# Kernel tuning notes

Hardware: AMD Instinct MI355X
Metric: run time of the kernel (lower is better)

## Reference

```python
import jax, jax.numpy as jnp
import numpy as np

B, T, D = 4, 2048, 2048
K, D_B, TOPK, WINDOW = 7, 128, 16, 64
GATE_CAP = 1.0
STRAND_CAP = 1.0
_PHI = 1.618033988749895
_PSI = -0.6180339887498949


def _ln(x, g, b, eps=1e-5):
    m = jnp.mean(x, axis=-1, keepdims=True)
    v = jnp.mean((x - m) ** 2, axis=-1, keepdims=True)
    return (x - m) * jax.lax.rsqrt(v + eps) * g + b


def setup_inputs() -> dict:
    ks = jax.random.split(jax.random.key(0), 20)
    rn = lambda k, s, sc=1.0: jax.random.normal(k, s, jnp.float32) * sc
    d_s = 1.0 / np.sqrt(D)
    db_s = 1.0 / np.sqrt(D_B)
    return {
        'X_write': rn(ks[0], (B, T, D)),
        'X_read': rn(ks[1], (B, T, D)),
        'slots': rn(ks[2], (B, K, D_B)),
        'W0': rn(ks[3], (D, D), d_s),
        'ln_write_g': jnp.ones((D,), jnp.float32),
        'ln_write_b': jnp.zeros((D,), jnp.float32),
        'Wv': rn(ks[4], (D_B, D), d_s),
        'Wk': rn(ks[5], (D_B, D_B), db_s),
        'slot_key_bias': rn(ks[6], (K, D_B), 2.0),
        'Wg_w': rn(ks[7], (D_B, 2 * D_B), 1.0 / np.sqrt(2 * D_B)),
        'Wg_b': jnp.full((D_B,), -2.0, jnp.float32),
        'ln_strand_g': jnp.ones((D_B,), jnp.float32),
        'ln_strand_b': jnp.zeros((D_B,), jnp.float32),
        'Wsq': rn(ks[8], (D_B, D_B), db_s),
        'Wsk': rn(ks[9], (D_B, D_B), db_s),
        'Wsv': rn(ks[10], (D_B, D_B), db_s),
        'lambda_strand': rn(ks[11], (D_B,), 0.1),
        'Wq_read': rn(ks[12], (D_B, D), d_s),
        'Wk_read': rn(ks[13], (D_B, D_B), db_s),
        'Wv_read': rn(ks[14], (D, D_B), db_s),
        'render_coeffs': rn(ks[15], (K, 3, D), 0.1),
        'slot_temps': 1.0 + rn(ks[16], (K,), 0.1),
    }


def reference(X_write, X_read, slots, W0, ln_write_g, ln_write_b, Wv, Wk,
              slot_key_bias, Wg_w, Wg_b, ln_strand_g, ln_strand_b,
              Wsq, Wsk, Wsv, lambda_strand, Wq_read, Wk_read, Wv_read,
              render_coeffs, slot_temps):
    b, t, d = X_write.shape
    sd = 1.0 / np.sqrt(D_B)
    X_n = _ln(X_write, ln_write_g, ln_write_b)

    # --- banded salience + topk (torch.no_grad region; only int indices escape) ---
    W_eff = min(WINDOW, t - 1)
    Xs = jax.lax.stop_gradient(X_n)
    X_W0 = Xs @ jax.lax.stop_gradient(W0).T            # [b,t,d]
    Xp = jnp.pad(X_W0, ((0, 0), (W_eff, 0), (0, 0)))   # left-pad so offset w -> j = i + w - W

    def band_dot(w):
        return jnp.einsum('btd,btd->bt', Xs,
                          jax.lax.dynamic_slice_in_dim(Xp, w, t, axis=1))

    band = jax.vmap(band_dot)(jnp.arange(W_eff)).transpose(1, 2, 0)  # [b,t,W]
    ii = jnp.arange(t)[:, None]
    ww = jnp.arange(W_eff)[None, :]
    jj = ii + ww - W_eff
    valid = (jj >= 0) & (ii >= 1)                      # j in [max(0,i-W), i)
    sal = jnp.where(valid, band, -jnp.inf).reshape(b, -1)
    topk_eff = min(TOPK, t * (t - 1) // 2)
    _, idx = jax.lax.top_k(sal, topk_eff)              # [b,topk]
    i_idx = idx // W_eff
    j_idx = i_idx + (idx % W_eff) - W_eff

    # --- topk pair gather + bilinear relation ---
    x_new = jnp.take_along_axis(X_n, i_idx[..., None], axis=1)  # [b,topk,d]
    x_old = jnp.take_along_axis(X_n, j_idx[..., None], axis=1)
    pair_sal = jnp.sum(x_new * (x_old @ jax.lax.stop_gradient(W0).T), axis=-1)
    alpha = jax.nn.softmax(pair_sal, axis=-1)
    R_t = jnp.einsum('bp,bpe->be', alpha, (x_new - x_old) @ Wv.T)  # [b,d_b]

    # --- slot write ---
    slot_keys = slots @ Wk.T + slot_key_bias[None]
    compat = jnp.einsum('bke,be->bk', slot_keys, R_t) * sd
    compat = compat * jax.nn.softplus(slot_temps)[None]
    sw = jax.nn.softmax(compat, axis=-1)
    weighted_R = sw[..., None] * R_t[:, None, :]                 # [b,K,d_b]
    g = jax.nn.sigmoid(jnp.concatenate([slots, weighted_R], -1) @ Wg_w.T + Wg_b)
    slots_upd = (1.0 - g) * slots + g * weighted_R

    # --- strand mixer (KxK self-attention) ---
    B_ln = _ln(slots_upd, ln_strand_g, ln_strand_b)
    att = jax.nn.softmax(jnp.einsum('bke,bme->bkm', B_ln @ Wsq.T, B_ln @ Wsk.T) * sd, axis=-1)
    ctx = att @ (B_ln @ Wsv.T)
    slots_next = slots_upd + ctx * jnp.clip(jnp.tanh(lambda_strand), -STRAND_CAP, STRAND_CAP)

    # --- aux losses ---
    L_persist = jnp.mean((slots_next - slots) ** 2)
    nrm = jnp.linalg.norm(slots_next, axis=-1, keepdims=True)
    Bn = slots_next / jnp.maximum(nrm, 1e-12)
    cos = jnp.einsum('bke,bme->bkm', Bn, Bn)
    off = 1.0 - jnp.eye(K, dtype=cos.dtype)
    L_div = jnp.sum(cos ** 2 * off) / (b * K * (K - 1))

    # --- directional render gate + read ---
    q_r = X_read @ Wq_read.T                    # [b,t,d_b]
    k_r = slots_next @ Wk_read.T                # [b,K,d_b]
    v_r = slots_next @ Wv_read.T                # [b,K,d]
    scores = jnp.einsum('bte,bke->btk', q_r, k_r) * sd
    q_mean = jnp.mean(X_read, axis=1)           # [b,d]
    w0q = q_mean @ jax.lax.stop_gradient(W0).T
    dphi = _PHI - _PSI
    phi_q = (w0q - _PSI * q_mean) / dphi
    psi_q = (_PHI * q_mean - w0q) / dphi
    pm = jnp.linalg.norm(phi_q, axis=-1, keepdims=True)
    sm = jnp.linalg.norm(psi_q, axis=-1, keepdims=True)
    tot = pm + sm + 1e-6
    basis = jnp.concatenate([jnp.ones_like(pm), pm / tot, sm / tot], axis=-1)  # [b,3]
    gate = jnp.clip(jnp.tanh(jnp.einsum('bi,kid->bkd', basis, render_coeffs)),
                    -GATE_CAP, GATE_CAP)
    z = jnp.einsum('btk,bkd->btd', jax.nn.softmax(scores, axis=-1), v_r * gate)
    return z, slots_next, L_persist, L_div
```

## Files before the change

kernel.cpp:

```cpp
#include <hip/hip_runtime.h>
#include <cstdint>
#include <cstddef>

#define DEV __device__ __forceinline__

typedef __bf16 bf16x8 __attribute__((ext_vector_type(8)));
typedef float f32x4 __attribute__((ext_vector_type(4)));
typedef unsigned short u16;
typedef unsigned int u32;

constexpr int Bq = 4, Tq = 2048, Dq = 2048, Kq = 7, DB = 128, TK = 16;
constexpr float SD = 0.08838834764831845f;
constexpr float PHIc = 1.618033988749895f;
constexpr float PSIc = -0.6180339887498949f;
constexpr float DPHI = 2.2360679774997896f;
#define NEG_INF (-__builtin_inff())

DEV u16 f2bf(float f) {
  union { float f; u32 u; } x; x.f = f;
  u32 r = (x.u + 0x7fffu + ((x.u >> 16) & 1u)) >> 16;
  return (u16)r;
}
DEV float bfbits2f(u32 h) { union { u32 u; float f; } x; x.u = h << 16; return x.f; }

DEV void async16(void* l, const void* g) {
  __builtin_amdgcn_global_load_lds((const __attribute__((address_space(1))) void*)g,
                                   (__attribute__((address_space(3))) void*)l, 16, 0, 0);
}

__global__ __launch_bounds__(256) void k_prep(const float* __restrict__ W0, u16* __restrict__ W0b,
                                              const float* __restrict__ Xw, const float* __restrict__ g,
                                              const float* __restrict__ bb, u16* __restrict__ Xn,
                                              const float* __restrict__ Xr, float* __restrict__ part) {
  int bid = blockIdx.x;
  int tid = threadIdx.x;
  if (bid < 2048) {
    size_t i = ((size_t)bid * 256 + tid) * 8;
    float4 a = *(const float4*)&W0[i];
    float4 c = *(const float4*)&W0[i + 4];
    u32 p0 = (u32)f2bf(a.x) | ((u32)f2bf(a.y) << 16);
    u32 p1 = (u32)f2bf(a.z) | ((u32)f2bf(a.w) << 16);
    u32 p2 = (u32)f2bf(c.x) | ((u32)f2bf(c.y) << 16);
    u32 p3 = (u32)f2bf(c.z) | ((u32)f2bf(c.w) << 16);
    uint4 st; st.x = p0; st.y = p1; st.z = p2; st.w = p3;
    *(uint4*)&W0b[i] = st;
  } else if (bid < 2048 + 8192) {
    int row = bid - 2048;
    const float* xr = Xw + (size_t)row * Dq;
    int lane = tid & 63, w = tid >> 6;
    float4 a = *(const float4*)&xr[tid * 8];
    float4 c = *(const float4*)&xr[tid * 8 + 4];
    float s = a.x + a.y + a.z + a.w + c.x + c.y + c.z + c.w;
    float q = a.x*a.x + a.y*a.y + a.z*a.z + a.w*a.w + c.x*c.x + c.y*c.y + c.z*c.z + c.w*c.w;
    #pragma unroll
    for (int o = 32; o; o >>= 1) { s += __shfl_xor(s, o); q += __shfl_xor(q, o); }
    __shared__ float red[8];
    if (lane == 0) { red[w] = s; red[w + 4] = q; }
    __syncthreads();
    float S = red[0] + red[1] + red[2] + red[3];
    float Q = red[4] + red[5] + red[6] + red[7];
    float mean = S * (1.0f / Dq);
    float var = Q * (1.0f / Dq) - mean * mean;
    float rstd = rsqrtf(var + 1e-5f);
    float v[8] = {a.x, a.y, a.z, a.w, c.x, c.y, c.z, c.w};
    u32 p[4];
    #pragma unroll
    for (int j = 0; j < 4; ++j) {
      int d0 = tid * 8 + j * 2;
      float o0 = (v[j*2]   - mean) * rstd * g[d0]   + bb[d0];
      float o1 = (v[j*2+1] - mean) * rstd * g[d0+1] + bb[d0+1];
      p[j] = (u32)f2bf(o0) | ((u32)f2bf(o1) << 16);
    }
    uint4 st; st.x = p[0]; st.y = p[1]; st.z = p[2]; st.w = p[3];
    *(uint4*)&Xn[(size_t)row * Dq + tid * 8] = st;
  } else {
    int f = bid - (2048 + 8192);
    int s = f & 1, y = (f >> 1) & 31, b = f >> 6;
    const float* xb = Xr + (size_t)b * Tq * Dq + (size_t)s * 1024 + tid * 4;
    f32x4 acc = {0.f, 0.f, 0.f, 0.f};
    #pragma unroll 4
    for (int t = 0; t < 64; ++t) {
      const float4 v = *(const float4*)&xb[(size_t)(y * 64 + t) * Dq];
      acc[0] += v.x; acc[1] += v.y; acc[2] += v.z; acc[3] += v.w;
    }
    float4 st; st.x = acc[0]; st.y = acc[1]; st.z = acc[2]; st.w = acc[3];
    *(float4*)&part[((size_t)(b * 32 + y)) * Dq + s * 1024 + tid * 4] = st;
  }
}

__global__ __launch_bounds__(256) void k_qmean2(const float* __restrict__ part, float* __restrict__ qm) {
  int s = blockIdx.x, b = blockIdx.y, tid = threadIdx.x;
  int col = s * 1024 + tid * 4;
  f32x4 acc = {0.f, 0.f, 0.f, 0.f};
  #pragma unroll 8
  for (int y = 0; y < 32; ++y) {
    float4 v = *(const float4*)&part[((size_t)(b * 32 + y)) * Dq + col];
    acc[0] += v.x; acc[1] += v.y; acc[2] += v.z; acc[3] += v.w;
  }
  float4 st;
  st.x = acc[0] * (1.0f / Tq); st.y = acc[1] * (1.0f / Tq);
  st.z = acc[2] * (1.0f / Tq); st.w = acc[3] * (1.0f / Tq);
  *(float4*)&qm[(size_t)b * Dq + col] = st;
}

__global__ __launch_bounds__(256) void k_w0q(const float* __restrict__ W0, const float* __restrict__ qm,
                                             float* __restrict__ w0q) {
  __shared__ float qs[4][Dq];
  int tid = threadIdx.x, lane = tid & 63, w = tid >> 6;
  for (int i = tid * 4; i < 4 * Dq; i += 1024) {
    *(float4*)&((float*)qs)[i] = *(const float4*)&qm[i];
  }
  __syncthreads();
  #pragma unroll
  for (int r = 0; r < 2; ++r) {
    int d = blockIdx.x * 8 + w * 2 + r;
    const float* wr = W0 + (size_t)d * Dq;
    float a0 = 0, a1 = 0, a2 = 0, a3 = 0;
    for (int e = lane * 4; e < Dq; e += 256) {
      float4 wv = *(const float4*)&wr[e];
      float4 q0 = *(const float4*)&qs[0][e];
      float4 q1 = *(const float4*)&qs[1][e];
      float4 q2 = *(const float4*)&qs[2][e];
      float4 q3 = *(const float4*)&qs[3][e];
      a0 += wv.x*q0.x + wv.y*q0.y + wv.z*q0.z + wv.w*q0.w;
      a1 += wv.x*q1.x + wv.y*q1.y + wv.z*q1.z + wv.w*q1.w;
      a2 += wv.x*q2.x + wv.y*q2.y + wv.z*q2.z + wv.w*q2.w;
      a3 += wv.x*q3.x + wv.y*q3.y + wv.z*q3.z + wv.w*q3.w;
    }
    #pragma unroll
    for (int o = 32; o; o >>= 1) {
      a0 += __shfl_xor(a0, o); a1 += __shfl_xor(a1, o);
      a2 += __shfl_xor(a2, o); a3 += __shfl_xor(a3, o);
    }
    if (lane == 0) {
      w0q[0 * Dq + d] = a0; w0q[1 * Dq + d] = a1;
      w0q[2 * Dq + d] = a2; w0q[3 * Dq + d] = a3;
    }
  }
}

__global__ __launch_bounds__(256) void k_basis(const float* __restrict__ qm, const float* __restrict__ w0q,
                                               float* __restrict__ basis) {
  int b = blockIdx.x, tid = threadIdx.x;
  __shared__ float red[256];
  __shared__ float psum;
  float ps = 0, ss = 0;
  for (int d = tid; d < Dq; d += 256) {
    float qv = qm[b * Dq + d], wv = w0q[b * Dq + d];
    float ph = (wv - PSIc * qv) * (1.0f / DPHI);
    float pv = (PHIc * qv - wv) * (1.0f / DPHI);
    ps += ph * ph; ss += pv * pv;
  }
  red[tid] = ps; __syncthreads();
  for (int st = 128; st; st >>= 1) { if (tid < st) red[tid] += red[tid + st]; __syncthreads(); }
  if (tid == 0) psum = red[0];
  __syncthreads();
  red[tid] = ss; __syncthreads();
  for (int st = 128; st; st >>= 1) { if (tid < st) red[tid] += red[tid + st]; __syncthreads(); }
  if (tid == 0) {
    float pm = sqrtf(psum), sm = sqrtf(red[0]);
    float tot = pm + sm + 1e-6f;
    basis[b * 3 + 0] = 1.0f; basis[b * 3 + 1] = pm / tot; basis[b * 3 + 2] = sm / tot;
  }
}

__global__ __launch_bounds__(256) void k_gemm(const u16* __restrict__ A, const u16* __restrict__ B,
                                              u16* __restrict__ C, int M, int N, int K) {
  __shared__ u16 As[128 * 64], Bs[128 * 64];
  int tid = threadIdx.x, lane = tid & 63, w = tid >> 6, wr = w >> 1, wc = w & 1;
  int bm = blockIdx.x, bn = blockIdx.y;
  const u16* Ab = A + (size_t)bm * 128 * K;
  const u16* Bb = B + (size_t)bn * 128 * K;
  f32x4 zero = {0.f, 0.f, 0.f, 0.f};
  f32x4 acc[4][4];
  #pragma unroll
  for (int mi = 0; mi < 4; ++mi)
    #pragma unroll
    for (int ni = 0; ni < 4; ++ni) acc[mi][ni] = zero;
  int ro = tid >> 3;
  int co = (tid & 7) * 8;
  int cs = co ^ ((ro & 7) * 8);
  for (int k0 = 0; k0 < K; k0 += 64) {
    #pragma unroll
    for (int i = 0; i < 4; ++i) {
      int row = ro + i * 32;
      async16(&As[row * 64 + co], Ab + (size_t)row * K + k0 + cs);
      async16(&Bs[row * 64 + co], Bb + (size_t)row * K + k0 + cs);
    }
    __syncthreads();
    #pragma unroll
    for (int ks = 0; ks < 2; ++ks) {
      int cbase = ks * 32 + ((lane >> 4) * 8);
      int crd = cbase ^ ((lane & 7) * 8);
      bf16x8 af[4], bfr[4];
      #pragma unroll
      for (int mi = 0; mi < 4; ++mi)
        af[mi] = *(const bf16x8*)&As[(wr * 64 + mi * 16 + (lane & 15)) * 64 + crd];
      #pragma unroll
      for (int ni = 0; ni < 4; ++ni)
        bfr[ni] = *(const bf16x8*)&Bs[(wc * 64 + ni * 16 + (lane & 15)) * 64 + crd];
      #pragma unroll
      for (int mi = 0; mi < 4; ++mi)
        #pragma unroll
        for (int ni = 0; ni < 4; ++ni)
          acc[mi][ni] = __builtin_amdgcn_mfma_f32_16x16x32_bf16(af[mi], bfr[ni], acc[mi][ni], 0, 0, 0);
    }
    __syncthreads();
  }
  int r0 = bm * 128 + wr * 64, c0 = bn * 128 + wc * 64;
  #pragma unroll
  for (int mi = 0; mi < 4; ++mi)
    #pragma unroll
    for (int ni = 0; ni < 4; ++ni) {
      int col = c0 + ni * 16 + (lane & 15);
      int rb = r0 + mi * 16 + ((lane >> 4) * 4);
      #pragma unroll
      for (int rg = 0; rg < 4; ++rg)
        C[(size_t)(rb + rg) * N + col] = f2bf(acc[mi][ni][rg]);
    }
}

__global__ __launch_bounds__(768) void k_band(const u16* __restrict__ Xn, const u16* __restrict__ XW0,
                                              float* __restrict__ sal) {
  int b = blockIdx.y, i0 = blockIdx.x * 32;
  int tid = threadIdx.x, lane = tid & 63, w = tid >> 6;
  int mi = w / 6, ni = w % 6;
  const u16* Xb = Xn + (size_t)b * Tq * Dq;
  const u16* Wb = XW0 + (size_t)b * Tq * Dq;
  int koff = (lane >> 4) * 8;
  const u16* ap = Xb + (size_t)(i0 + mi * 16 + (lane & 15)) * Dq + koff;
  int j = i0 - 64 + ni * 16 + (lane & 15); j = min(max(j, 0), Tq - 1);
  const u16* bp = Wb + (size_t)j * Dq + koff;
  f32x4 zero = {0.f, 0.f, 0.f, 0.f};
  f32x4 accA = zero, accB = zero;
  for (int k = 0; k < Dq; k += 64) {
    bf16x8 a0 = *(const bf16x8*)(ap + k);
    bf16x8 b0 = *(const bf16x8*)(bp + k);
    bf16x8 a1 = *(const bf16x8*)(ap + k + 32);
    bf16x8 b1 = *(const bf16x8*)(bp + k + 32);
    accA = __builtin_amdgcn_mfma_f32_16x16x32_bf16(a0, b0, accA, 0, 0, 0);
    accB = __builtin_amdgcn_mfma_f32_16x16x32_bf16(a1, b1, accB, 0, 0, 0);
  }
  int nl = ni * 16 + (lane & 15);
  #pragma unroll
  for (int rg = 0; rg < 4; ++rg) {
    int i = i0 + mi * 16 + (lane >> 4) * 4 + rg;
    int wb = nl - (i - i0);
    if (wb >= 0 && wb < 64) {
      int jj = i0 - 64 + nl;
      bool valid = (jj >= 0) && (i >= 1);
      sal[((size_t)b * Tq + i) * 64 + wb] = valid ? (accA[rg] + accB[rg]) : NEG_INF;
    }
  }
}

__global__ __launch_bounds__(256) void k_topk1(const float* __restrict__ sal,
                                               float* __restrict__ cv, int* __restrict__ ci) {
  int b = blockIdx.y, chunk = blockIdx.x;
  int tid = threadIdx.x, lane = tid & 63;
  const float* s = sal + (size_t)b * Tq * 64 + (size_t)chunk * 1024;
  float lv[4]; int li[4];
  #pragma unroll
  for (int i = 0; i < 4; ++i) { lv[i] = NEG_INF; li[i] = -1; }
  #pragma unroll
  for (int i = 0; i < 4; ++i) {
    int e = tid + i * 256;
    float v = s[e];
    int idx = chunk * 1024 + e;
    if (v > lv[3]) {
      lv[3] = v; li[3] = idx;
      #pragma unroll
      for (int q = 3; q > 0; --q)
        if (lv[q] > lv[q - 1]) {
          float tv = lv[q]; lv[q] = lv[q - 1]; lv[q - 1] = tv;
          int t2 = li[q]; li[q] = li[q - 1]; li[q - 1] = t2;
        }
    }
  }
  __shared__ float Sv[256][4];
  __shared__ int Si[256][4];
  __shared__ int heads[256];
  #pragma unroll
  for (int i = 0; i < 4; ++i) { Sv[tid][i] = lv[i]; Si[tid][i] = li[i]; }
  heads[tid] = 0;
  __syncthreads();
  float* ov = cv + ((size_t)b * 128 + chunk) * 16;
  int* oi = ci + ((size_t)b * 128 + chunk) * 16;
  for (int r = 0; r < 16; ++r) {
    if (tid < 64) {
      float best = NEG_INF; int bl = 0; int bidx = 0x7fffffff;
      #pragma unroll
      for (int cc = 0; cc < 4; ++cc) {
        int c = lane + cc * 64;
        int h = heads[c];
        float v = (h < 4) ? Sv[c][h] : NEG_INF;
        int ix = (h < 4) ? Si[c][h] : 0x7fffffff;
        if (v > best || (v == best && ix < bidx)) { best = v; bl = c; bidx = ix; }
      }
      #pragma unroll
      for (int o = 32; o; o >>= 1) {
        float bv = __shfl_xor(best, o); int blx = __shfl_xor(bl, o); int bix = __shfl_xor(bidx, o);
        if (bv > best || (bv == best && bix < bidx)) { best = bv; bl = blx; bidx = bix; }
      }
      if (lane == 0) {
        int h = heads[bl];
        ov[r] = best; oi[r] = (h < 4) ? Si[bl][h] : -1;
        heads[bl] = h + 1;
      }
    }
    __syncthreads();
  }
}

__global__ __launch_bounds__(256) void k_topk2(const float* __restrict__ cv, const int* __restrict__ ci,
                                               int* __restrict__ ti, int* __restrict__ tj) {
  int b = blockIdx.x, tid = threadIdx.x, lane = tid & 63;
  __shared__ float Sv[128][16];
  __shared__ int Si[128][16];
  __shared__ int heads[128];
  __shared__ int ridx[16];
  for (int i = tid; i < 128 * 16; i += 256) {
    ((float*)Sv)[i] = cv[(size_t)b * 2048 + i];
    ((int*)Si)[i] = ci[(size_t)b * 2048 + i];
  }
  if (tid < 128) heads[tid] = 0;
  __syncthreads();
  for (int r = 0; r < 16; ++r) {
    if (tid < 64) {
      float best = NEG_INF; int bl = 0; int bidx = 0x7fffffff;
      #pragma unroll
      for (int cc = 0; cc < 2; ++cc) {
        int c = lane + cc * 64;
        int h = heads[c];
        float v = (h < 16) ? Sv[c][h] : NEG_INF;
        int ix = (h < 16) ? Si[c][h] : 0x7fffffff;
        if (v > best || (v == best && ix < bidx)) { best = v; bl = c; bidx = ix; }
      }
      #pragma unroll
      for (int o = 32; o; o >>= 1) {
        float bv = __shfl_xor(best, o); int blx = __shfl_xor(bl, o); int bix = __shfl_xor(bidx, o);
        if (bv > best || (bv == best && bix < bidx)) { best = bv; bl = blx; bidx = bix; }
      }
// ... 52 lines not shown
}

__global__ __launch_bounds__(256) void k_pairsal(const float* __restrict__ W0, const float* __restrict__ Xnew,
                                                 const float* __restrict__ Xold, float* __restrict__ psal) {
  int d0 = blockIdx.x * 64, e0 = blockIdx.y * 64;
  int tid = threadIdx.x, P = tid & 63, dg = tid >> 6;
  f32x4 xo[16];
  #pragma unroll
  for (int i = 0; i < 16; ++i)
    xo[i] = *(const f32x4*)&Xold[(size_t)P * Dq + e0 + i * 4];
  int dbase = d0 + dg * 16;
  f32x4 xn[4];
  #pragma unroll
  for (int i = 0; i < 4; ++i)
    xn[i] = *(const f32x4*)&Xnew[(size_t)P * Dq + dbase + i * 4];
  float acc = 0.f;
  #pragma unroll
  for (int dd = 0; dd < 16; ++dd) {
    int d = __builtin_amdgcn_readfirstlane(dbase + dd);
    const float* wr = W0 + (size_t)d * Dq + e0;
    float i0 = 0.f, i1 = 0.f, i2 = 0.f, i3 = 0.f;
    #pragma unroll
    for (int i = 0; i < 16; ++i) {
      float4 wv = *(const float4*)&wr[i * 4];
      i0 += wv.x * xo[i][0]; i1 += wv.y * xo[i][1];
      i2 += wv.z * xo[i][2]; i3 += wv.w * xo[i][3];
    }
    acc += xn[dd >> 2][dd & 3] * ((i0 + i1) + (i2 + i3));
  }
  __shared__ float part[4][64];
  part[dg][P] = acc;
  __syncthreads();
  if (tid < 64)
    atomicAdd(&psal[tid], part[0][tid] + part[1][tid] + part[2][tid] + part[3][tid]);
}

__global__ __launch_bounds__(256) void k_alphart(const float* __restrict__ psal, const float* __restrict__ Xnew,
    const float* __restrict__ Xold, const float* __restrict__ Wv, float* __restrict__ Rt) {
  int bx = blockIdx.x, b = blockIdx.y;
  int tid = threadIdx.x, lane = tid & 63, w = tid >> 6;
  __shared__ float al[16], xd[Dq];
  if (tid == 0) {
    float mx = NEG_INF;
    #pragma unroll
    for (int p = 0; p < 16; ++p) mx = fmaxf(mx, psal[b * 16 + p]);
    float ee[16]; float s = 0.f;
    #pragma unroll
    for (int p = 0; p < 16; ++p) { ee[p] = expf(psal[b * 16 + p] - mx); s += ee[p]; }
    #pragma unroll
    for (int p = 0; p < 16; ++p) al[p] = ee[p] / s;
  }
  __syncthreads();
  {
    int d0 = tid * 8;
    float a8[8] = {0, 0, 0, 0, 0, 0, 0, 0};
    #pragma unroll
    for (int p = 0; p < 16; ++p) {
      const float* xn = Xnew + (size_t)(b * 16 + p) * Dq + d0;
      const float* xo = Xold + (size_t)(b * 16 + p) * Dq + d0;
      float ap = al[p];
      float4 n0 = *(const float4*)xn;
      float4 n1 = *(const float4*)(xn + 4);
      float4 o0 = *(const float4*)xo;
      float4 o1 = *(const float4*)(xo + 4);
      a8[0] += ap * (n0.x - o0.x); a8[1] += ap * (n0.y - o0.y);
      a8[2] += ap * (n0.z - o0.z); a8[3] += ap * (n0.w - o0.w);
      a8[4] += ap * (n1.x - o1.x); a8[5] += ap * (n1.y - o1.y);
      a8[6] += ap * (n1.z - o1.z); a8[7] += ap * (n1.w - o1.w);
    }
    #pragma unroll
    for (int j = 0; j < 8; ++j) xd[d0 + j] = a8[j];
  }
  __syncthreads();
  int e = bx * 4 + w;
  const float* wr = Wv + (size_t)e * Dq;
  float s = 0.f;
  #pragma unroll 8
  for (int d = lane; d < Dq; d += 64) s += wr[d] * xd[d];
  #pragma unroll
  for (int o = 32; o; o >>= 1) s += __shfl_xor(s, o);
  if (lane == 0) Rt[b * DB + e] = s;
}

__global__ __launch_bounds__(256) void ksl_a(const float* __restrict__ slots, const float* __restrict__ Wk,
    const float* __restrict__ skb, const float* __restrict__ Rt, const float* __restrict__ temps,
    float* __restrict__ compat) {
  int k = blockIdx.x, b = blockIdx.y;
  int tid = threadIdx.x, g = tid >> 4, sub = tid & 15;
  __shared__ float s_s[DB], r_s[DB], sk_s[DB];
  if (tid < DB) { s_s[tid] = slots[((size_t)(b * Kq + k)) * DB + tid]; r_s[tid] = Rt[b * DB + tid]; }
  __syncthreads();
  #pragma unroll
  for (int r = 0; r < 8; ++r) {
    int e = g * 8 + r;
    const float* wr = Wk + e * DB;
    float a = 0.f;
    #pragma unroll
    for (int j = 0; j < 8; ++j) a += wr[sub + j * 16] * s_s[sub + j * 16];
    a += __shfl_xor(a, 8); a += __shfl_xor(a, 4); a += __shfl_xor(a, 2); a += __shfl_xor(a, 1);
    if (sub == 0) sk_s[e] = a + skb[k * DB + e];
  }
  __syncthreads();
  if (tid < 64) {
    float a = sk_s[tid] * r_s[tid] + sk_s[tid + 64] * r_s[tid + 64];
    #pragma unroll
    for (int o = 32; o; o >>= 1) a += __shfl_xor(a, o);
    if (tid == 0) {
      float t = temps[k];
      compat[b * Kq + k] = a * SD * log1pf(expf(t));
    }
  }
}

__global__ __launch_bounds__(256) void ksl_c(const float* __restrict__ slots, const float* __restrict__ Rt,
    const float* __restrict__ compat, const float* __restrict__ Wgw, const float* __restrict__ Wgb,
    const float* __restrict__ lng, const float* __restrict__ lnb,
    const float* __restrict__ Wsq, const float* __restrict__ Wsk, const float* __restrict__ Wsv,
    float* __restrict__ suOut, float* __restrict__ qqOut, float* __restrict__ kkOut,
    float* __restrict__ vvOut) {
  int k = blockIdx.x, b = blockIdx.y;
  int tid = threadIdx.x, g = tid >> 4, sub = tid & 15;
  __shared__ float s_s[DB], r_s[DB], su[DB], bnl[DB];
  __shared__ float mvm, mvr;
  if (tid < DB) { s_s[tid] = slots[((size_t)(b * Kq + k)) * DB + tid]; r_s[tid] = Rt[b * DB + tid]; }
  __syncthreads();
  float swk;
  {
    float cm[Kq]; float mx = NEG_INF;
    #pragma unroll
    for (int kk = 0; kk < Kq; ++kk) { cm[kk] = compat[b * Kq + kk]; mx = fmaxf(mx, cm[kk]); }
    float ssum = 0.f;
    #pragma unroll
    for (int kk = 0; kk < Kq; ++kk) { cm[kk] = expf(cm[kk] - mx); ssum += cm[kk]; }
    swk = cm[k] / ssum;
  }
  #pragma unroll
  for (int r = 0; r < 8; ++r) {
    int e = g * 8 + r;
    const float* wr = Wgw + e * 256;
    float a = 0.f;
    #pragma unroll
    for (int j = 0; j < 16; ++j) {
      int col = sub + j * 16;
      float x = (j < 8) ? s_s[col] : swk * r_s[col - 128];
      a += wr[col] * x;
    }
    a += __shfl_xor(a, 8); a += __shfl_xor(a, 4); a += __shfl_xor(a, 2); a += __shfl_xor(a, 1);
    if (sub == 0) {
      a += Wgb[e];
      float gv = 1.0f / (1.0f + expf(-a));
      float wrv = swk * r_s[e];
      su[e] = (1.0f - gv) * s_s[e] + gv * wrv;
    }
  }
  __syncthreads();
  if (tid < 64) {
    float v0 = su[tid], v1 = su[tid + 64];
    float s = v0 + v1, q = v0 * v0 + v1 * v1;
    #pragma unroll
    for (int o = 32; o; o >>= 1) { s += __shfl_xor(s, o); q += __shfl_xor(q, o); }
    if (tid == 0) {
      float m = s / DB; float va = q / DB - m * m;
      mvm = m; mvr = rsqrtf(va + 1e-5f);
    }
  }
  __syncthreads();
  if (tid < DB) {
    bnl[tid] = (su[tid] - mvm) * mvr * lng[tid] + lnb[tid];
    suOut[((size_t)(b * Kq + k)) * DB + tid] = su[tid];
  }
  __syncthreads();
  #pragma unroll
  for (int r = 0; r < 8; ++r) {
    int e = g * 8 + r;
    const float* wr1 = Wsq + e * DB;
    const float* wr2 = Wsk + e * DB;
    const float* wr3 = Wsv + e * DB;
    float a1 = 0.f, a2 = 0.f, a3 = 0.f;
    #pragma unroll
    for (int j = 0; j < 8; ++j) {
      float x = bnl[sub + j * 16];
      a1 += wr1[sub + j * 16] * x;
      a2 += wr2[sub + j * 16] * x;
      a3 += wr3[sub + j * 16] * x;
    }
    #pragma unroll
    for (int o = 8; o; o >>= 1) {
      a1 += __shfl_xor(a1, o); a2 += __shfl_xor(a2, o); a3 += __shfl_xor(a3, o);
    }
    if (sub == 0) {
      size_t oi = ((size_t)(b * Kq + k)) * DB + e;
      qqOut[oi] = a1; kkOut[oi] = a2; vvOut[oi] = a3;
    }
  }
}

__global__ __launch_bounds__(256) void ksl_d(const float* __restrict__ suOut, const float* __restrict__ qqOut,
    const float* __restrict__ kkOut, const float* __restrict__ vvOut, const float* __restrict__ lam,
    const float* __restrict__ Wkr, float* __restrict__ snOut, float* __restrict__ krOut) {
  int k = blockIdx.x, b = blockIdx.y;
  int tid = threadIdx.x, g = tid >> 4, sub = tid & 15;
  __shared__ float qq[DB], kks[Kq][DB], vvs[Kq][DB], att[8], sn_s[DB];
  if (tid < DB) qq[tid] = qqOut[((size_t)(b * Kq + k)) * DB + tid];
  for (int i = tid; i < Kq * DB; i += 256) {
    ((float*)kks)[i] = kkOut[(size_t)b * Kq * DB + i];
    ((float*)vvs)[i] = vvOut[(size_t)b * Kq * DB + i];
  }
  __syncthreads();
  if (tid < 112) {
    int m = g;
    float a = 0.f;
    #pragma unroll
    for (int j = 0; j < 8; ++j) a += qq[sub + j * 16] * kks[m][sub + j * 16];
    a += __shfl_xor(a, 8); a += __shfl_xor(a, 4); a += __shfl_xor(a, 2); a += __shfl_xor(a, 1);
    if (sub == 0) att[m] = a * SD;
  }
  __syncthreads();
  if (tid == 0) {
    float mx = att[0];
    for (int m = 1; m < Kq; ++m) mx = fmaxf(mx, att[m]);
    float s = 0.f;
    for (int m = 0; m < Kq; ++m) { att[m] = expf(att[m] - mx); s += att[m]; }
    for (int m = 0; m < Kq; ++m) att[m] /= s;
  }
  __syncthreads();
  if (tid < DB) {
    float c = 0.f;
    #pragma unroll
    for (int m = 0; m < Kq; ++m) c += att[m] * vvs[m][tid];
    float l = tanhf(lam[tid]); l = fminf(fmaxf(l, -1.0f), 1.0f);
    float v = suOut[((size_t)(b * Kq + k)) * DB + tid] + c * l;
    sn_s[tid] = v;
    snOut[((size_t)(b * Kq + k)) * DB + tid] = v;
  }
  __syncthreads();
  #pragma unroll
  for (int r = 0; r < 8; ++r) {
    int e = g * 8 + r;
    const float* wr = Wkr + e * DB;
    float a = 0.f;
    #pragma unroll
    for (int j = 0; j < 8; ++j) a += wr[sub + j * 16] * sn_s[sub + j * 16];
    a += __shfl_xor(a, 8); a += __shfl_xor(a, 4); a += __shfl_xor(a, 2); a += __shfl_xor(a, 1);
    if (sub == 0) krOut[((size_t)(b * Kq + k)) * DB + e] = a;
  }
}

__global__ __launch_bounds__(256) void k_mvg(const float* __restrict__ snOut, const float* __restrict__ krOut,
    const float* __restrict__ Wqr, const float* __restrict__ Wvr, const float* __restrict__ rc,
    const float* __restrict__ basis, const float* __restrict__ slots,
    u16* __restrict__ Mb, u16* __restrict__ Vgb, float* __restrict__ out2) {
  int b = blockIdx.y, tid = threadIdx.x;
  if (blockIdx.x == 8) {
    if (b != 0) return;
    __shared__ float red[256];
    __shared__ float nrm[28];
    float p = 0.f;
    for (int i = tid; i < Bq * Kq * DB; i += 256) { float d = snOut[i] - slots[i]; p += d * d; }
    red[tid] = p; __syncthreads();
    for (int st = 128; st; st >>= 1) { if (tid < st) red[tid] += red[tid + st]; __syncthreads(); }
    if (tid == 0) out2[0] = red[0] / (float)(Bq * Kq * DB);
    if (tid < 28) {
      int bb2 = tid / 7, k = tid % 7;
      float s = 0.f;
      for (int e = 0; e < DB; ++e) { float v = snOut[(size_t)(bb2 * 7 + k) * DB + e]; s += v * v; }
      nrm[tid] = fmaxf(sqrtf(s), 1e-12f);
    }
    __syncthreads();
    float dv = 0.f;
    if (tid < 168) {
      int bb2 = tid / 42, r = tid % 42;
      int k = r / 6, m = r % 6; m += (m >= k);
      float dot = 0.f;
      for (int e = 0; e < DB; ++e)
        dot += snOut[(size_t)(bb2 * 7 + k) * DB + e] * snOut[(size_t)(bb2 * 7 + m) * DB + e];
      float c = dot / (nrm[bb2 * 7 + k] * nrm[bb2 * 7 + m]);
      dv = c * c;
    }
    red[tid] = dv; __syncthreads();
    for (int st = 128; st; st >>= 1) { if (tid < st) red[tid] += red[tid + st]; __syncthreads(); }
    if (tid == 0) out2[1] = red[0] / 168.0f;
    return;
  }
  int d = blockIdx.x * 256 + tid;
  __shared__ float krs[Kq][DB], sns[Kq][DB];
  for (int i = tid; i < Kq * DB; i += 256) {
    ((float*)krs)[i] = krOut[(size_t)b * Kq * DB + i];
    ((float*)sns)[i] = snOut[(size_t)b * Kq * DB + i];
  }
  __syncthreads();
  float b0 = basis[b * 3 + 0], b1 = basis[b * 3 + 1], b2 = basis[b * 3 + 2];
  float am[7] = {0, 0, 0, 0, 0, 0, 0};
  for (int e = 0; e < DB; ++e) {
    float wq = Wqr[(size_t)e * Dq + d];
    #pragma unroll
    for (int k = 0; k < 7; ++k) am[k] += krs[k][e] * wq;
  }
  float vr[7] = {0, 0, 0, 0, 0, 0, 0};
  const float* wvrow = Wvr + (size_t)d * DB;
  for (int e = 0; e < DB; ++e) {
    float wv = wvrow[e];
    #pragma unroll
    for (int k = 0; k < 7; ++k) vr[k] += sns[k][e] * wv;
  }
  #pragma unroll
  for (int k = 0; k < 7; ++k) {
    Mb[((size_t)b * 7 + k) * Dq + d] = f2bf(am[k]);
    float gt = tanhf(b0 * rc[((size_t)k * 3 + 0) * Dq + d] +
                     b1 * rc[((size_t)k * 3 + 1) * Dq + d] +
                     b2 * rc[((size_t)k * 3 + 2) * Dq + d]);
    gt = fminf(fmaxf(gt, -1.0f), 1.0f);
    Vgb[((size_t)b * 7 + k) * Dq + d] = f2bf(vr[k] * gt);
  }
}
// ... 22 lines not shown
    #pragma unroll
    for (int k = 0; k < 7; ++k) {
      #pragma unroll
      for (int o = 32; o; o >>= 1) sc[k] += __shfl_xor(sc[k], o);
    }
    float mx = sc[0];
    #pragma unroll
    for (int k = 1; k < 7; ++k) mx = fmaxf(mx, sc[k]);
    float pz[7]; float s = 0.f;
    #pragma unroll
    for (int k = 0; k < 7; ++k) { pz[k] = expf((sc[k] - mx) * SD); s += pz[k]; }
    float inv = 1.0f / s;
    #pragma unroll
    for (int k = 0; k < 7; ++k) pz[k] *= inv;
    float* zr = Z + ((size_t)b * Tq + t) * Dq;
    #pragma unroll
    for (int i = 0; i < 8; ++i) {
      int d = lane * 4 + i * 256;
      float4 o4; o4.x = o4.y = o4.z = o4.w = 0.f;
      #pragma unroll
      for (int k = 0; k < 7; ++k) {
        uint2 vm = *(const uint2*)&Vs[k * 2048 + d];
        float pk = pz[k];
        o4.x += pk * bfbits2f(vm.x & 0xffffu); o4.y += pk * bfbits2f(vm.x >> 16);
        o4.z += pk * bfbits2f(vm.y & 0xffffu); o4.w += pk * bfbits2f(vm.y >> 16);
      }
      *(float4*)&zr[d] = o4;
    }
  }
}

extern "C" void kernel_launch(void* const* d_in, const int* in_sizes, int n_in,
                              void* d_out, int out_size, void* d_ws, size_t ws_size,
                              hipStream_t stream) {
  const float* Xw   = (const float*)d_in[0];
  const float* Xr   = (const float*)d_in[1];
  const float* slots= (const float*)d_in[2];
  const float* W0   = (const float*)d_in[3];
  const float* lng  = (const float*)d_in[4];
  const float* lnb  = (const float*)d_in[5];
  const float* Wv   = (const float*)d_in[6];
  const float* Wk   = (const float*)d_in[7];
  const float* skb  = (const float*)d_in[8];
  const float* Wgw  = (const float*)d_in[9];
  const float* Wgb  = (const float*)d_in[10];
  const float* lsg  = (const float*)d_in[11];
  const float* lsb  = (const float*)d_in[12];
  const float* Wsq  = (const float*)d_in[13];
  const float* Wsk  = (const float*)d_in[14];
  const float* Wsv  = (const float*)d_in[15];
  const float* lam  = (const float*)d_in[16];
  const float* Wqr  = (const float*)d_in[17];
  const float* Wkr  = (const float*)d_in[18];
  const float* Wvr  = (const float*)d_in[19];
  const float* rc   = (const float*)d_in[20];
  const float* temps= (const float*)d_in[21];

  char* wsb = (char*)d_ws;
  size_t off = 0;
  auto alloc = [&](size_t bytes) -> void* {
    void* p = wsb + off;
    off += (bytes + 255) & ~(size_t)255;
    return p;
  };
  u16*   Xn   = (u16*)  alloc((size_t)Bq * Tq * Dq * 2);
  u16*   XW0  = (u16*)  alloc((size_t)Bq * Tq * Dq * 2);
  u16*   W0b  = (u16*)  alloc((size_t)Dq * Dq * 2);
  float* sal  = (float*)alloc((size_t)Bq * Tq * 64 * 4);
  int*   ti   = (int*)  alloc(Bq * TK * 4);
  int*   tj   = (int*)  alloc(Bq * TK * 4);
  float* Xnew = (float*)alloc((size_t)Bq * TK * Dq * 4);
  float* Xold = (float*)alloc((size_t)Bq * TK * Dq * 4);
  float* psal = (float*)alloc(Bq * TK * 4);
  float* Rt   = (float*)alloc(Bq * DB * 4);
  float* qm   = (float*)alloc(Bq * Dq * 4);
  float* w0q  = (float*)alloc(Bq * Dq * 4);
  float* basis= (float*)alloc(Bq * 3 * 4);
  float* krOut= (float*)alloc(Bq * Kq * DB * 4);
  u16*   Mbf  = (u16*)  alloc((size_t)Bq * Kq * Dq * 2);
  u16*   Vgb  = (u16*)  alloc((size_t)Bq * Kq * Dq * 2);
  float* cv   = (float*)alloc((size_t)Bq * 128 * 16 * 4);
  int*   ci   = (int*)  alloc((size_t)Bq * 128 * 16 * 4);
  float* part = (float*)alloc((size_t)Bq * 32 * Dq * 4);
  float* compat = (float*)alloc(Bq * Kq * 4);
  float* suB  = (float*)alloc(Bq * Kq * DB * 4);
  float* qqB  = (float*)alloc(Bq * Kq * DB * 4);
  float* kkB  = (float*)alloc(Bq * Kq * DB * 4);
  float* vvB  = (float*)alloc(Bq * Kq * DB * 4);

  float* Zout = (float*)d_out;
  float* snOut = Zout + (size_t)Bq * Tq * Dq;
  float* lossOut = snOut + Bq * Kq * DB;

  k_prep  <<<2048 + 8192 + 256, 256, 0, stream>>>(W0, W0b, Xw, lng, lnb, Xn, Xr, part);
  k_qmean2<<<dim3(2, Bq), 256, 0, stream>>>(part, qm);
  k_w0q   <<<256, 256, 0, stream>>>(W0, qm, w0q);
  k_basis <<<Bq, 256, 0, stream>>>(qm, w0q, basis);
  k_gemm  <<<dim3(64, 16), 256, 0, stream>>>(Xn, W0b, XW0, Bq * Tq, Dq, Dq);
  k_band  <<<dim3(64, Bq), 768, 0, stream>>>(Xn, XW0, sal);
  k_topk1 <<<dim3(128, Bq), 256, 0, stream>>>(sal, cv, ci);
  k_topk2 <<<Bq, 256, 0, stream>>>(cv, ci, ti, tj);
  k_gatherln<<<dim3(32, Bq), 256, 0, stream>>>(Xw, lng, lnb, ti, tj, Xnew, Xold, psal);
  k_pairsal<<<dim3(32, 32), 256, 0, stream>>>(W0, Xnew, Xold, psal);
  k_alphart<<<dim3(32, Bq), 256, 0, stream>>>(psal, Xnew, Xold, Wv, Rt);
  ksl_a   <<<dim3(Kq, Bq), 256, 0, stream>>>(slots, Wk, skb, Rt, temps, compat);
  ksl_c   <<<dim3(Kq, Bq), 256, 0, stream>>>(slots, Rt, compat, Wgw, Wgb, lsg, lsb,
                                             Wsq, Wsk, Wsv, suB, qqB, kkB, vvB);
  ksl_d   <<<dim3(Kq, Bq), 256, 0, stream>>>(suB, qqB, kkB, vvB, lam, Wkr, snOut, krOut);
  k_mvg   <<<dim3(9, Bq), 256, 0, stream>>>(snOut, krOut, Wqr, Wvr, rc, basis, slots,
                                            Mbf, Vgb, lossOut);
  k_z     <<<dim3(128, Bq), 256, 0, stream>>>(Xr, Mbf, Vgb, Zout);
}
```

Before: 404.2 us.

## Fold small q-mean/basis kernels into gemm/band/topk and merge slot kernels

Result: slower. 467.8 us (+15.7%).

```diff
diff --git a/kernel.cpp b/kernel.cpp
--- a/kernel.cpp
+++ b/kernel.cpp
@@ -88,86 +88,29 @@
   }
 }
 
-__global__ __launch_bounds__(256) void k_qmean2(const float* __restrict__ part, float* __restrict__ qm) {
-  int s = blockIdx.x, b = blockIdx.y, tid = threadIdx.x;
-  int col = s * 1024 + tid * 4;
-  f32x4 acc = {0.f, 0.f, 0.f, 0.f};
-  #pragma unroll 8
-  for (int y = 0; y < 32; ++y) {
-    float4 v = *(const float4*)&part[((size_t)(b * 32 + y)) * Dq + col];
-    acc[0] += v.x; acc[1] += v.y; acc[2] += v.z; acc[3] += v.w;
-  }
-  float4 st;
-  st.x = acc[0] * (1.0f / Tq); st.y = acc[1] * (1.0f / Tq);
-  st.z = acc[2] * (1.0f / Tq); st.w = acc[3] * (1.0f / Tq);
-  *(float4*)&qm[(size_t)b * Dq + col] = st;
-}
-
-__global__ __launch_bounds__(256) void k_w0q(const float* __restrict__ W0, const float* __restrict__ qm,
-                                             float* __restrict__ w0q) {
-  __shared__ float qs[4][Dq];
-  int tid = threadIdx.x, lane = tid & 63, w = tid >> 6;
-  for (int i = tid * 4; i < 4 * Dq; i += 1024) {
-    *(float4*)&((float*)qs)[i] = *(const float4*)&qm[i];
-  }
-  __syncthreads();
-  #pragma unroll
-  for (int r = 0; r < 2; ++r) {
-    int d = blockIdx.x * 8 + w * 2 + r;
-    const float* wr = W0 + (size_t)d * Dq;
-    float a0 = 0, a1 = 0, a2 = 0, a3 = 0;
-    for (int e = lane * 4; e < Dq; e += 256) {
-      float4 wv = *(const float4*)&wr[e];
-      float4 q0 = *(const float4*)&qs[0][e];
-      float4 q1 = *(const float4*)&qs[1][e];
-      float4 q2 = *(const float4*)&qs[2][e];
-      float4 q3 = *(const float4*)&qs[3][e];
-      a0 += wv.x*q0.x + wv.y*q0.y + wv.z*q0.z + wv.w*q0.w;
-      a1 += wv.x*q1.x + wv.y*q1.y + wv.z*q1.z + wv.w*q1.w;
-      a2 += wv.x*q2.x + wv.y*q2.y + wv.z*q2.z + wv.w*q2.w;
-      a3 += wv.x*q3.x + wv.y*q3.y + wv.z*q3.z + wv.w*q3.w;
-    }
-    #pragma unroll
-    for (int o = 32; o; o >>= 1) {
-      a0 += __shfl_xor(a0, o); a1 += __shfl_xor(a1, o);
-      a2 += __shfl_xor(a2, o); a3 += __shfl_xor(a3, o);
-    }
-    if (lane == 0) {
-      w0q[0 * Dq + d] = a0; w0q[1 * Dq + d] = a1;
-      w0q[2 * Dq + d] = a2; w0q[3 * Dq + d] = a3;
-    }
-  }
-}
-
-__global__ __launch_bounds__(256) void k_basis(const float* __restrict__ qm, const float* __restrict__ w0q,
-                                               float* __restrict__ basis) {
-  int b = blockIdx.x, tid = threadIdx.x;
-  __shared__ float red[256];
-  __shared__ float psum;
-  float ps = 0, ss = 0;
-  for (int d = tid; d < Dq; d += 256) {
-    float qv = qm[b * Dq + d], wv = w0q[b * Dq + d];
-    float ph = (wv - PSIc * qv) * (1.0f / DPHI);
-    float pv = (PHIc * qv - wv) * (1.0f / DPHI);
-    ps += ph * ph; ss += pv * pv;
-  }
-  red[tid] = ps; __syncthreads();
-  for (int st = 128; st; st >>= 1) { if (tid < st) red[tid] += red[tid + st]; __syncthreads(); }
-  if (tid == 0) psum = red[0];
-  __syncthreads();
-  red[tid] = ss; __syncthreads();
-  for (int st = 128; st; st >>= 1) { if (tid < st) red[tid] += red[tid + st]; __syncthreads(); }
-  if (tid == 0) {
-    float pm = sqrtf(psum), sm = sqrtf(red[0]);
-    float tot = pm + sm + 1e-6f;
-    basis[b * 3 + 0] = 1.0f; basis[b * 3 + 1] = pm / tot; basis[b * 3 + 2] = sm / tot;
-  }
-}
-
 __global__ __launch_bounds__(256) void k_gemm(const u16* __restrict__ A, const u16* __restrict__ B,
-                                              u16* __restrict__ C, int M, int N, int K) {
+                                              u16* __restrict__ C, int M, int N, int K,
+                                              const float* __restrict__ part, float* __restrict__ qm) {
   __shared__ u16 As[128 * 64], Bs[128 * 64];
-  int tid = threadIdx.x, lane = tid & 63, w = tid >> 6, wr = w >> 1, wc = w & 1;
+  int tid = threadIdx.x;
+  if (blockIdx.y == 16) {
+    int bm = blockIdx.x;
+    if (bm >= 8) return;
+    int s = bm & 1, b = bm >> 1;
+    int col = s * 1024 + tid * 4;
+    f32x4 acc = {0.f, 0.f, 0.f, 0.f};
+    #pragma unroll 8
+    for (int y = 0; y < 32; ++y) {
+      float4 v = *(const float4*)&part[((size_t)(b * 32 + y)) * Dq + col];
+      acc[0] += v.x; acc[1] += v.y; acc[2] += v.z; acc[3] += v.w;
+    }
+    float4 st;
+    st.x = acc[0] * (1.0f / Tq); st.y = acc[1] * (1.0f / Tq);
+    st.z = acc[2] * (1.0f / Tq); st.w = acc[3] * (1.0f / Tq);
+    *(float4*)&qm[(size_t)b * Dq + col] = st;
+    return;
+  }
+  int lane = tid & 63, w = tid >> 6, wr = w >> 1, wc = w & 1;
   int bm = blockIdx.x, bn = blockIdx.y;
   const u16* Ab = A + (size_t)bm * 128 * K;
   const u16* Bb = B + (size_t)bn * 128 * K;
@@ -221,9 +164,40 @@
 }
 
 __global__ __launch_bounds__(768) void k_band(const u16* __restrict__ Xn, const u16* __restrict__ XW0,
-                                              float* __restrict__ sal) {
+                                              float* __restrict__ sal,
+                                              const float* __restrict__ W0, const float* __restrict__ qm,
+                                              float* __restrict__ w0q) {
+  int tid = threadIdx.x, lane = tid & 63, w = tid >> 6;
+  if (blockIdx.y == Bq) {
+    int x = blockIdx.x;
+    for (int r = w; r < 32; r += 12) {
+      int d = x * 32 + r;
+      const float* wr = W0 + (size_t)d * Dq;
+      float a0 = 0, a1 = 0, a2 = 0, a3 = 0;
+      for (int e = lane * 4; e < Dq; e += 256) {
+        float4 wv = *(const float4*)&wr[e];
+        float4 q0 = *(const float4*)&qm[0 * Dq + e];
+        float4 q1 = *(const float4*)&qm[1 * Dq + e];
+        float4 q2 = *(const float4*)&qm[2 * Dq + e];
+        float4 q3 = *(const float4*)&qm[3 * Dq + e];
+        a0 += wv.x*q0.x + wv.y*q0.y + wv.z*q0.z + wv.w*q0.w;
+        a1 += wv.x*q1.x + wv.y*q1.y + wv.z*q1.z + wv.w*q1.w;
+        a2 += wv.x*q2.x + wv.y*q2.y + wv.z*q2.z + wv.w*q2.w;
+        a3 += wv.x*q3.x + wv.y*q3.y + wv.z*q3.z + wv.w*q3.w;
+      }
+      #pragma unroll
+      for (int o = 32; o; o >>= 1) {
+        a0 += __shfl_xor(a0, o); a1 += __shfl_xor(a1, o);
+        a2 += __shfl_xor(a2, o); a3 += __shfl_xor(a3, o);
+      }
+      if (lane == 0) {
+        w0q[0 * Dq + d] = a0; w0q[1 * Dq + d] = a1;
+        w0q[2 * Dq + d] = a2; w0q[3 * Dq + d] = a3;
+      }
+    }
+    return;
+  }
   int b = blockIdx.y, i0 = blockIdx.x * 32;
-  int tid = threadIdx.x, lane = tid & 63, w = tid >> 6;
   int mi = w / 6, ni = w % 6;
   const u16* Xb = Xn + (size_t)b * Tq * Dq;
   const u16* Wb = XW0 + (size_t)b * Tq * Dq;
@@ -255,9 +229,34 @@
 }
 
 __global__ __launch_bounds__(256) void k_topk1(const float* __restrict__ sal,
-                                               float* __restrict__ cv, int* __restrict__ ci) {
-  int b = blockIdx.y, chunk = blockIdx.x;
-  int tid = threadIdx.x, lane = tid & 63;
+                                               float* __restrict__ cv, int* __restrict__ ci,
+                                               const float* __restrict__ qm, const float* __restrict__ w0q,
+                                               float* __restrict__ basis) {
+  int b = blockIdx.y, tid = threadIdx.x, lane = tid & 63;
+  if (blockIdx.x == 128) {
+    __shared__ float red[256];
+    __shared__ float psum;
+    float ps = 0, ss = 0;
+    for (int d = tid; d < Dq; d += 256) {
+      float qv = qm[b * Dq + d], wv = w0q[b * Dq + d];
+      float ph = (wv - PSIc * qv) * (1.0f / DPHI);
+      float pv = (PHIc * qv - wv) * (1.0f / DPHI);
+      ps += ph * ph; ss += pv * pv;
+    }
+    red[tid] = ps; __syncthreads();
+    for (int st = 128; st; st >>= 1) { if (tid < st) red[tid] += red[tid + st]; __syncthreads(); }
+    if (tid == 0) psum = red[0];
+    __syncthreads();
+    red[tid] = ss; __syncthreads();
+    for (int st = 128; st; st >>= 1) { if (tid < st) red[tid] += red[tid + st]; __syncthreads(); }
+    if (tid == 0) {
+      float pm = sqrtf(psum), sm = sqrtf(red[0]);
+      float tot = pm + sm + 1e-6f;
+      basis[b * 3 + 0] = 1.0f; basis[b * 3 + 1] = pm / tot; basis[b * 3 + 2] = sm / tot;
+    }
+    return;
+  }
+  int chunk = blockIdx.x;
   const float* s = sal + (size_t)b * Tq * 64 + (size_t)chunk * 1024;
   float lv[4]; int li[4];
   #pragma unroll
@@ -476,67 +475,63 @@
   if (lane == 0) Rt[b * DB + e] = s;
 }
 
-__global__ __launch_bounds__(256) void ksl_a(const float* __restrict__ slots, const float* __restrict__ Wk,
+__global__ __launch_bounds__(256) void k_slots2(const float* __restrict__ slots, const float* __restrict__ Wk,
     const float* __restrict__ skb, const float* __restrict__ Rt, const float* __restrict__ temps,
-    float* __restrict__ compat) {
+    const float* __restrict__ Wgw, const float* __restrict__ Wgb,
+    const float* __restrict__ lng, const float* __restrict__ lnb,
+    const float* __restrict__ Wsq, const float* __restrict__ Wsk, const float* __restrict__ Wsv,
+    const float* __restrict__ lam, const float* __restrict__ Wkr,
+    float* __restrict__ snOut, float* __restrict__ krOut) {
   int k = blockIdx.x, b = blockIdx.y;
   int tid = threadIdx.x, g = tid >> 4, sub = tid & 15;
-  __shared__ float s_s[DB], r_s[DB], sk_s[DB];
-  if (tid < DB) { s_s[tid] = slots[((size_t)(b * Kq + k)) * DB + tid]; r_s[tid] = Rt[b * DB + tid]; }
-  __syncthreads();
-  #pragma unroll
-  for (int r = 0; r < 8; ++r) {
-    int e = g * 8 + r;
+  __shared__ float s_all[Kq][DB], r_s[DB], skS[Kq][DB], su_all[Kq][DB], bnl_all[Kq][DB],
+                   kks[Kq][DB], vvs[Kq][DB], qqk[DB], sn_s[DB], cmS[8], att[8], mv[Kq][2];
+  for (int i = tid; i < Kq * DB; i += 256) ((float*)s_all)[i] = slots[(size_t)b * Kq * DB + i];
+  if (tid < DB) r_s[tid] = Rt[b * DB + tid];
+  __syncthreads();
+  for (int o = g; o < Kq * DB; o += 16) {
+    int kk = o >> 7, e = o & 127;
     const float* wr = Wk + e * DB;
     float a = 0.f;
     #pragma unroll
-    for (int j = 0; j < 8; ++j) a += wr[sub + j * 16] * s_s[sub + j * 16];
+    for (int j = 0; j < 8; ++j) a += wr[sub + j * 16] * s_all[kk][sub + j * 16];
     a += __shfl_xor(a, 8); a += __shfl_xor(a, 4); a += __shfl_xor(a, 2); a += __shfl_xor(a, 1);
-    if (sub == 0) sk_s[e] = a + skb[k * DB + e];
-  }
-  __syncthreads();
-  if (tid < 64) {
-    float a = sk_s[tid] * r_s[tid] + sk_s[tid + 64] * r_s[tid + 64];
-    #pragma unroll
-    for (int o = 32; o; o >>= 1) a += __shfl_xor(a, o);
-    if (tid == 0) {
-      float t = temps[k];
-      compat[b * Kq + k] = a * SD * log1pf(expf(t));
-    }
-  }
-}
-
-__global__ __launch_bounds__(256) void ksl_c(const float* __restrict__ slots, const float* __restrict__ Rt,
-    const float* __restrict__ compat, const float* __restrict__ Wgw, const float* __restrict__ Wgb,
-    const float* __restrict__ lng, const float* __restrict__ lnb,
-    const float* __restrict__ Wsq, const float* __restrict__ Wsk, const float* __restrict__ Wsv,
-    float* __restrict__ suOut, float* __restrict__ qqOut, float* __restrict__ kkOut,
-    float* __restrict__ vvOut) {
-  int k = blockIdx.x, b = blockIdx.y;
-  int tid = threadIdx.x, g = tid >> 4, sub = tid & 15;
-  __shared__ float s_s[DB], r_s[DB], su[DB], bnl[DB];
-  __shared__ float mvm, mvr;
-  if (tid < DB) { s_s[tid] = slots[((size_t)(b * Kq + k)) * DB + tid]; r_s[tid] = Rt[b * DB + tid]; }
-  __syncthreads();
-  float swk;
+    if (sub == 0) skS[kk][e] = a + skb[o];
+  }
+  __syncthreads();
+  if (tid < 112) {
+    int kk = g;
+    float a = 0.f;
+    #pragma unroll
+    for (int j = 0; j < 8; ++j) a += skS[kk][sub + j * 16] * r_s[sub + j * 16];
+    a += __shfl_xor(a, 8); a += __shfl_xor(a, 4); a += __shfl_xor(a, 2); a += __shfl_xor(a, 1);
+    if (sub == 0) {
+      float t = temps[kk];
+      cmS[kk] = a * SD * log1pf(expf(t));
+    }
+  }
+  __syncthreads();
+  float sw[Kq];
   {
-    float cm[Kq]; float mx = NEG_INF;
-    #pragma unroll
-    for (int kk = 0; kk < Kq; ++kk) { cm[kk] = compat[b * Kq + kk]; mx = fmaxf(mx, cm[kk]); }
+    float mx = NEG_INF;
+    #pragma unroll
+    for (int kk = 0; kk < Kq; ++kk) mx = fmaxf(mx, cmS[kk]);
     float ssum = 0.f;
     #pragma unroll
-    for (int kk = 0; kk < Kq; ++kk) { cm[kk] = expf(cm[kk] - mx); ssum += cm[kk]; }
-    swk = cm[k] / ssum;
-  }
-  #pragma unroll
-  for (int r = 0; r < 8; ++r) {
-    int e = g * 8 + r;
+    for (int kk = 0; kk < Kq; ++kk) { sw[kk] = expf(cmS[kk] - mx); ssum += sw[kk]; }
+    float inv = 1.0f / ssum;
+    #pragma unroll
+    for (int kk = 0; kk < Kq; ++kk) sw[kk] *= inv;
+  }
+  for (int o = g; o < Kq * DB; o += 16) {
+    int kk = o >> 7, e = o & 127;
     const float* wr = Wgw + e * 256;
+    float swk = sw[kk];
     float a = 0.f;
     #pragma unroll
     for (int j = 0; j < 16; ++j) {
       int col = sub + j * 16;
-      float x = (j < 8) ? s_s[col] : swk * r_s[col - 128];
+      float x = (j < 8) ? s_all[kk][col] : swk * r_s[col - 128];
       a += wr[col] * x;
     }
     a += __shfl_xor(a, 8); a += __shfl_xor(a, 4); a += __shfl_xor(a, 2); a += __shfl_xor(a, 1);
@@ -544,68 +539,59 @@
       a += Wgb[e];
       float gv = 1.0f / (1.0f + expf(-a));
       float wrv = swk * r_s[e];
-      su[e] = (1.0f - gv) * s_s[e] + gv * wrv;
-    }
-  }
-  __syncthreads();
-  if (tid < 64) {
-    float v0 = su[tid], v1 = su[tid + 64];
-    float s = v0 + v1, q = v0 * v0 + v1 * v1;
-    #pragma unroll
-    for (int o = 32; o; o >>= 1) { s += __shfl_xor(s, o); q += __shfl_xor(q, o); }
-    if (tid == 0) {
+      su_all[kk][e] = (1.0f - gv) * s_all[kk][e] + gv * wrv;
+    }
+  }
+  __syncthreads();
+  if (tid < 112) {
+    int kk = g;
+    float s = 0.f, q = 0.f;
+    #pragma unroll
+    for (int j = 0; j < 8; ++j) {
+      float v = su_all[kk][sub + j * 16];
+      s += v; q += v * v;
+    }
+    s += __shfl_xor(s, 8); s += __shfl_xor(s, 4); s += __shfl_xor(s, 2); s += __shfl_xor(s, 1);
+    q += __shfl_xor(q, 8); q += __shfl_xor(q, 4); q += __shfl_xor(q, 2); q += __shfl_xor(q, 1);
+    if (sub == 0) {
       float m = s / DB; float va = q / DB - m * m;
-      mvm = m; mvr = rsqrtf(va + 1e-5f);
-    }
-  }
-  __syncthreads();
-  if (tid < DB) {
-    bnl[tid] = (su[tid] - mvm) * mvr * lng[tid] + lnb[tid];
-    suOut[((size_t)(b * Kq + k)) * DB + tid] = su[tid];
-  }
-  __syncthreads();
-  #pragma unroll
-  for (int r = 0; r < 8; ++r) {
-    int e = g * 8 + r;
+      mv[kk][0] = m; mv[kk][1] = rsqrtf(va + 1e-5f);
+    }
+  }
+  __syncthreads();
+  for (int i = tid; i < Kq * DB; i += 256) {
+    int kk = i >> 7, e = i & 127;
+    bnl_all[kk][e] = (su_all[kk][e] - mv[kk][0]) * mv[kk][1] * lng[e] + lnb[e];
+  }
+  __syncthreads();
+  for (int o = g; o < Kq * DB; o += 16) {
+    int kk = o >> 7, e = o & 127;
     const float* wr1 = Wsq + e * DB;
     const float* wr2 = Wsk + e * DB;
     const float* wr3 = Wsv + e * DB;
     float a1 = 0.f, a2 = 0.f, a3 = 0.f;
     #pragma unroll
     for (int j = 0; j < 8; ++j) {
-      float x = bnl[sub + j * 16];
+      float x = bnl_all[kk][sub + j * 16];
       a1 += wr1[sub + j * 16] * x;
       a2 += wr2[sub + j * 16] * x;
       a3 += wr3[sub + j * 16] * x;
     }
     #pragma unroll
-    for (int o = 8; o; o >>= 1) {
-      a1 += __shfl_xor(a1, o); a2 += __shfl_xor(a2, o); a3 += __shfl_xor(a3, o);
+    for (int o2 = 8; o2; o2 >>= 1) {
+      a1 += __shfl_xor(a1, o2); a2 += __shfl_xor(a2, o2); a3 += __shfl_xor(a3, o2);
     }
     if (sub == 0) {
-      size_t oi = ((size_t)(b * Kq + k)) * DB + e;
-      qqOut[oi] = a1; kkOut[oi] = a2; vvOut[oi] = a3;
-    }
-  }
-}
-
-__global__ __launch_bounds__(256) void ksl_d(const float* __restrict__ suOut, const float* __restrict__ qqOut,
-    const float* __restrict__ kkOut, const float* __restrict__ vvOut, const float* __restrict__ lam,
-    const float* __restrict__ Wkr, float* __restrict__ snOut, float* __restrict__ krOut) {
-  int k = blockIdx.x, b = blockIdx.y;
-  int tid = threadIdx.x, g = tid >> 4, sub = tid & 15;
-  __shared__ float qq[DB], kks[Kq][DB], vvs[Kq][DB], att[8], sn_s[DB];
-  if (tid < DB) qq[tid] = qqOut[((size_t)(b * Kq + k)) * DB + tid];
-  for (int i = tid; i < Kq * DB; i += 256) {
-    ((float*)kks)[i] = kkOut[(size_t)b * Kq * DB + i];
-    ((float*)vvs)[i] = vvOut[(size_t)b * Kq * DB + i];
+      kks[kk][e] = a2; vvs[kk][e] = a3;
+      if (kk == k) qqk[e] = a1;
+    }
   }
   __syncthreads();
   if (tid < 112) {
     int m = g;
     float a = 0.f;
     #pragma unroll
-    for (int j = 0; j < 8; ++j) a += qq[sub + j * 16] * kks[m][sub + j * 16];
+    for (int j = 0; j < 8; ++j) a += qqk[sub + j * 16] * kks[m][sub + j * 16];
     a += __shfl_xor(a, 8); a += __shfl_xor(a, 4); a += __shfl_xor(a, 2); a += __shfl_xor(a, 1);
     if (sub == 0) att[m] = a * SD;
   }
@@ -623,7 +609,7 @@
     #pragma unroll
     for (int m = 0; m < Kq; ++m) c += att[m] * vvs[m][tid];
     float l = tanhf(lam[tid]); l = fminf(fmaxf(l, -1.0f), 1.0f);
-    float v = suOut[((size_t)(b * Kq + k)) * DB + tid] + c * l;
+    float v = su_all[k][tid] + c * l;
     sn_s[tid] = v;
     snOut[((size_t)(b * Kq + k)) * DB + tid] = v;
   }
@@ -812,31 +798,21 @@
   float* cv   = (float*)alloc((size_t)Bq * 128 * 16 * 4);
   int*   ci   = (int*)  alloc((size_t)Bq * 128 * 16 * 4);
   float* part = (float*)alloc((size_t)Bq * 32 * Dq * 4);
-  float* compat = (float*)alloc(Bq * Kq * 4);
-  float* suB  = (float*)alloc(Bq * Kq * DB * 4);
-  float* qqB  = (float*)alloc(Bq * Kq * DB * 4);
-  float* kkB  = (float*)alloc(Bq * Kq * DB * 4);
-  float* vvB  = (float*)alloc(Bq * Kq * DB * 4);
 
   float* Zout = (float*)d_out;
   float* snOut = Zout + (size_t)Bq * Tq * Dq;
   float* lossOut = snOut + Bq * Kq * DB;
 
   k_prep  <<<2048 + 8192 + 256, 256, 0, stream>>>(W0, W0b, Xw, lng, lnb, Xn, Xr, part);
-  k_qmean2<<<dim3(2, Bq), 256, 0, stream>>>(part, qm);
-  k_w0q   <<<256, 256, 0, stream>>>(W0, qm, w0q);
-  k_basis <<<Bq, 256, 0, stream>>>(qm, w0q, basis);
-  k_gemm  <<<dim3(64, 16), 256, 0, stream>>>(Xn, W0b, XW0, Bq * Tq, Dq, Dq);
-  k_band  <<<dim3(64, Bq), 768, 0, stream>>>(Xn, XW0, sal);
-  k_topk1 <<<dim3(128, Bq), 256, 0, stream>>>(sal, cv, ci);
+  k_gemm  <<<dim3(64, 17), 256, 0, stream>>>(Xn, W0b, XW0, Bq * Tq, Dq, Dq, part, qm);
+  k_band  <<<dim3(64, Bq + 1), 768, 0, stream>>>(Xn, XW0, sal, W0, qm, w0q);
+  k_topk1 <<<dim3(129, Bq), 256, 0, stream>>>(sal, cv, ci, qm, w0q, basis);
   k_topk2 <<<Bq, 256, 0, stream>>>(cv, ci, ti, tj);
   k_gatherln<<<dim3(32, Bq), 256, 0, stream>>>(Xw, lng, lnb, ti, tj, Xnew, Xold, psal);
   k_pairsal<<<dim3(32, 32), 256, 0, stream>>>(W0, Xnew, Xold, psal);
   k_alphart<<<dim3(32, Bq), 256, 0, stream>>>(psal, Xnew, Xold, Wv, Rt);
-  ksl_a   <<<dim3(Kq, Bq), 256, 0, stream>>>(slots, Wk, skb, Rt, temps, compat);
-  ksl_c   <<<dim3(Kq, Bq), 256, 0, stream>>>(slots, Rt, compat, Wgw, Wgb, lsg, lsb,
-                                             Wsq, Wsk, Wsv, suB, qqB, kkB, vvB);
-  ksl_d   <<<dim3(Kq, Bq), 256, 0, stream>>>(suB, qqB, kkB, vvB, lam, Wkr, snOut, krOut);
+  k_slots2<<<dim3(Kq, Bq), 256, 0, stream>>>(slots, Wk, skb, Rt, temps, Wgw, Wgb, lsg, lsb,
+                                             Wsq, Wsk, Wsv, lam, Wkr, snOut, krOut);
   k_mvg   <<<dim3(9, Bq), 256, 0, stream>>>(snOut, krOut, Wqr, Wvr, rc, basis, slots,
                                             Mbf, Vgb, lossOut);
   k_z     <<<dim3(128, Bq), 256, 0, stream>>>(Xr, Mbf, Vgb, Zout);
```
